# Performance work log

Measured on AMD Instinct MI355X. Metric: run time of the kernel, lower is better.

## Reference

```python
import jax, jax.numpy as jnp
import numpy as np

B = 2
NUM_CLS = 20
NUM_DIM = 256
H = W = 448
FH = FW = 28
K_TOP = 25


def _l2norm(x, eps=1e-12):
    # matches torch F.normalize(dim=1): x / max(||x||, eps); zero rows stay zero
    return x / jnp.maximum(jnp.linalg.norm(x, axis=-1, keepdims=True), eps)


def setup_inputs():
    key = jax.random.key(0)
    k1, k2, k3, k4 = jax.random.split(key, 4)
    fmap = jax.random.normal(k1, (B, NUM_DIM, FH, FW), jnp.float32)
    cam = jax.random.uniform(k2, (B, NUM_CLS, H, W), jnp.float32)
    cls_label = jax.random.randint(k3, (B, NUM_CLS), 0, 2).astype(jnp.float32)
    proj_weight = jax.random.normal(k4, (NUM_CLS, NUM_DIM), jnp.float32) * 0.02
    feature_contrast = jnp.zeros((NUM_CLS, NUM_DIM), jnp.float32)
    return {"fmap": fmap, "cam": cam, "cls_label": cls_label,
            "proj_weight": proj_weight, "feature_contrast": feature_contrast,
            "hig_thre": 0.7, "low_thre": 0.25, "bg_thre": 0.5}


def _forward(fmap, cam, cls_label, proj_weight, feature_contrast, hig_thre, low_thre, bg_thre):
    b, c, h, w = cam.shape
    d = fmap.shape[1]
    dt = fmap.dtype

    # ---- pseudo-label generation (vectorized over b,h,w) ----
    valid_cam = cls_label[:, :, None, None] * cam                       # [B,C,H,W]
    top2_v, top2_i = jax.lax.top_k(jnp.moveaxis(valid_cam, 1, -1), 2)   # [B,H,W,2]
    top1, second = top2_v[..., 0], top2_v[..., 1]
    pseudo = top2_i[..., 0] + 1
    pseudo = jnp.where(top1 < hig_thre, 255, pseudo)
    pseudo = jnp.where(top1 < low_thre, 0, pseudo)
    pseudo = jnp.where(top1 < bg_thre, 0, pseudo)
    pseudo = jnp.where((top1 - second < 0.3) & (top1 > hig_thre), 255, pseudo)

    # ---- upsample features (bilinear, align_corners=False) ----
    fmap_up = jax.image.resize(fmap, (b, d, h, w), 'bilinear')
    fmap_flat = fmap_up.reshape(b, d, h * w)                            # [B,D,HW]
    pseudo_flat = pseudo.reshape(b, h * w)                              # [B,HW]

    # ---- per-class features, both branches computed densely then selected ----
    cls_ids = jnp.arange(c) + 1
    mask = (pseudo_flat[:, None, :] == cls_ids[None, :, None]).astype(dt)  # [B,C,HW]
    counts = mask.sum(-1)                                                  # [B,C]
    feat_mask = jnp.einsum('bcp,bdp->bcd', mask, fmap_flat) / jnp.maximum(counts, 1.0)[:, :, None]
    _, top_idx = jax.lax.top_k(valid_cam.reshape(b, c, h * w), K_TOP)      # [B,C,25]
    gathered = jnp.take_along_axis(fmap_flat[:, None, :, :], top_idx[:, :, None, :], axis=-1)  # [B,C,D,25]
    feat_topk = gathered.mean(-1)                                          # [B,C,D]
    present = cls_label > 0.5                                              # [B,C] bool
    fsm = jnp.where((counts == 0.0)[:, :, None], feat_topk, feat_mask) * present[:, :, None]

    eye_f = jnp.eye(c, dtype=dt)
    eye_b = jnp.eye(c, dtype=bool)

    # ---- sequential per-sample loop (EMA memory bank carried across batch) ----
    def step(carry, xs):
        fc, loss_cls, loss_ccf = carry
        fsm_i, present_i = xs                                    # [C,D], [C]
        fsm_n = _l2norm(fsm_i)
        fc_n = _l2norm(jax.lax.stop_gradient(fc))
        cos = jnp.clip(jnp.abs(fsm_n @ fc_n.T), 1e-5, 1.0 - 1e-5)  # [C,C]
        ident = jnp.diag(present_i.astype(dt))
        loss_ccf = loss_ccf - (ident * jnp.log(cos) + (1.0 - ident) * jnp.log1p(-cos)).mean()
        off_max = jnp.where(eye_b, -jnp.inf, cos).max(axis=1)      # max over j != c
        qualify = present_i & (off_max < 0.6)                      # [C] bool
        p = jax.nn.softmax(fsm_i @ proj_weight.T, axis=-1)         # [C,C]
        logp = jnp.maximum(jnp.log(p), -100.0)
        log1mp = jnp.maximum(jnp.log1p(-p), -100.0)
        term = -(eye_f * logp + (1.0 - eye_f) * log1mp).mean(axis=-1)  # BCE(softmax, onehot) per class
        loss_cls = loss_cls + jnp.sum(jnp.where(qualify, term, 0.0))
        n = qualify.sum().astype(dt)
        loss_cls = jnp.where(n > 0, loss_cls / jnp.maximum(n, 1.0), loss_cls)
        fc = jnp.where(qualify[:, None], 0.95 * fc + 0.05 * jax.lax.stop_gradient(fsm_i), fc)
        return (fc, loss_cls, loss_ccf), None

    zero = jnp.asarray(0.0, dt)
    (_, loss_cls, loss_ccf), _ = jax.lax.scan(step, (feature_contrast, zero, zero), (fsm, present))
    return loss_ccf + loss_cls


def reference(fmap, cam, cls_label, proj_weight, feature_contrast, hig_thre, low_thre, bg_thre):
    return _forward(fmap, cam, cls_label, proj_weight, feature_contrast, hig_thre, low_thre, bg_thre)
```

## Files before the change

### kernel.cpp

```cpp
#include <hip/hip_runtime.h>
#include <cstdint>

#define HW 200704
#define IMG_W 448
#define NCLS 20
#define NDIM 256
#define NB2 784
#define LK 260

#define ASYNC_COPY16(gp, lp)                                                   \
  __builtin_amdgcn_global_load_lds(                                            \
      (const __attribute__((address_space(1))) void*)(gp),                     \
      (__attribute__((address_space(3))) void*)(lp), 16, 0, 0)

__global__ __launch_bounds__(256) void k_front(const float* __restrict__ fmap,
                                               float* __restrict__ fmapT,
                                               const float* __restrict__ cam,
                                               const float* __restrict__ cls_label,
                                               const float* __restrict__ hig_p,
                                               const float* __restrict__ low_p,
                                               const float* __restrict__ bg_p,
                                               float* __restrict__ W) {
  __shared__ float sT[NCLS][256];
  __shared__ int presList[NCLS];
  __shared__ int sNP;
  int tid = threadIdx.x;

  if (blockIdx.x >= 2 * NB2) {
    float (*tile)[33] = (float (*)[33]) & sT[0][0];
    int blk = blockIdx.x - 2 * NB2;
    int b = blk / 200;
    int t = blk % 200;
    int dT = t / 25, sT2 = t % 25;
    int ty = tid >> 5, tx = tid & 31;
#pragma unroll
    for (int r = 0; r < 4; ++r) {
      int d = dT * 32 + ty + r * 8;
      int s = sT2 * 32 + tx;
      if (s < 784) tile[ty + r * 8][tx] = fmap[((size_t)(b * 256 + d)) * 784 + s];
    }
    __syncthreads();
#pragma unroll
    for (int r = 0; r < 4; ++r) {
      int s = sT2 * 32 + ty + r * 8;
      int d = dT * 32 + tx;
      if (s < 784) fmapT[((size_t)(b * 784 + s)) * 256 + d] = tile[tx][ty + r * 8];
    }
    return;
  }

  int b = blockIdx.x / NB2;
  int blkInB = blockIdx.x % NB2;
  int pix0 = blkInB * 256;
  int wave = tid >> 6, lane = tid & 63;

  if (tid < 64) {
    bool pres = (tid < NCLS) && (cls_label[b * NCLS + tid] != 0.0f);
    unsigned long long pm = __ballot(pres);
    if (pres) presList[(int)__popcll(pm & ((1ull << tid) - 1ull))] = tid;
    if (tid == 0) sNP = (int)__popcll(pm);
  }
  __syncthreads();
  int np = sNP;
  const float* camb = cam + (size_t)b * NCLS * HW + pix0;

  for (int k = wave; k < np; k += 4)
    ASYNC_COPY16(camb + (size_t)presList[k] * HW + lane * 4, &sT[k][0]);
  __syncthreads();

  float top1 = -1.0f, sec = -1.0f;
  int cls1 = 0;
  for (int k = 0; k < np; ++k) {
    float x = sT[k][tid];
    bool gt = x > top1;
    sec = gt ? top1 : fmaxf(sec, fminf(x, top1));
    cls1 = gt ? presList[k] : cls1;
    top1 = gt ? x : top1;
  }
  if (np < NCLS) sec = fmaxf(sec, 0.0f);
  float hig = hig_p[0], low = low_p[0], bg = bg_p[0];
  int pix = pix0 + tid;
  int ps = cls1 + 1;
  if (top1 < hig) ps = 255;
  if (top1 < low) ps = 0;
  if (top1 < bg)  ps = 0;
  if ((top1 - sec < 0.3f) && (top1 > hig)) ps = 255;
  if (ps >= 1 && ps <= NCLS) {
    int cls = ps - 1;
    int y = pix / IMG_W, x = pix % IMG_W;
    float sy = (y + 0.5f) * 0.0625f - 0.5f; sy = fminf(fmaxf(sy, 0.0f), 27.0f);
    float sx = (x + 0.5f) * 0.0625f - 0.5f; sx = fminf(fmaxf(sx, 0.0f), 27.0f);
    int fy0 = (int)sy, fx0 = (int)sx;
    int fy1 = min(fy0 + 1, 27), fx1 = min(fx0 + 1, 27);
    float wy = sy - (float)fy0, wx = sx - (float)fx0;
    float* Wb = W + (size_t)(b * NCLS + cls) * 784;
    atomicAdd(&Wb[fy0 * 28 + fx0], (1.0f - wy) * (1.0f - wx));
    atomicAdd(&Wb[fy0 * 28 + fx1], (1.0f - wy) * wx);
    atomicAdd(&Wb[fy1 * 28 + fx0], wy * (1.0f - wx));
    atomicAdd(&Wb[fy1 * 28 + fx1], wy * wx);
  }
}

__global__ __launch_bounds__(1024) void k_feat_loss(const float* __restrict__ fmapT,
                                                    const float* __restrict__ cam,
                                                    const float* __restrict__ Wg,
                                                    const float* __restrict__ cls_label,
                                                    const float* __restrict__ proj_w,
                                                    const float* __restrict__ fc_init,
                                                    int* __restrict__ done,
                                                    float* __restrict__ fsm_g,
                                                    float* __restrict__ out) {
  __shared__ float sW[784];
  __shared__ float sPart[4][256];
  __shared__ float wv[16]; __shared__ int wi[16];
  __shared__ float selV; __shared__ int selI;
  __shared__ int sTop[25];
  __shared__ int sLast;
  __shared__ float sRed[16];
  __shared__ float sCntf;
  __shared__ float sFsm[NCLS * LK], sFc[NCLS * LK], sPw[NCLS * LK];
  __shared__ float sMat[NCLS * NCLS], sRow[NCLS], sNormI[NCLS], sNormC[NCLS];
  __shared__ int   sZI[NCLS], sZC[NCLS], sQual[NCLS];
  __shared__ float sPres[2][NCLS];
  __shared__ float sScal[2];

  int bc = blockIdx.x;
  int b = bc / NCLS;
  int tid = threadIdx.x;
  int dim = tid & 255, part = tid >> 8;
  bool present = (cls_label[bc] != 0.0f);
  const float* fT = fmapT + (size_t)b * 784 * 256;
  float res = 0.0f;

  if (present) {
    for (int s = tid; s < 784; s += 1024) sW[s] = Wg[(size_t)bc * 784 + s];
    __syncthreads();
    {
      float cs = (tid < 784) ? sW[tid] : 0.0f;
      for (int off = 32; off > 0; off >>= 1) cs += __shfl_xor(cs, off, 64);
      if ((tid & 63) == 0) sRed[tid >> 6] = cs;
      __syncthreads();
      if (tid == 0) {
        float s = 0.0f;
        for (int w = 0; w < 16; ++w) s += sRed[w];
        sCntf = s;
      }
      __syncthreads();
    }
    float cntf = sCntf;
    if (cntf > 0.0f) {
      float a0 = 0.0f, a1 = 0.0f, a2 = 0.0f, a3 = 0.0f;
      int s0 = part * 196;
      for (int s = s0; s < s0 + 196; s += 4) {
        a0 += sW[s]     * fT[(size_t)(s)     * 256 + dim];
        a1 += sW[s + 1] * fT[(size_t)(s + 1) * 256 + dim];
        a2 += sW[s + 2] * fT[(size_t)(s + 2) * 256 + dim];
        a3 += sW[s + 3] * fT[(size_t)(s + 3) * 256 + dim];
      }
      sPart[part][dim] = (a0 + a1) + (a2 + a3);
      __syncthreads();
      if (tid < 256)
        res = ((sPart[0][tid] + sPart[1][tid]) + (sPart[2][tid] + sPart[3][tid]))
              / fmaxf(cntf, 1.0f);
    } else {
      const float* camc = cam + (size_t)bc * HW;
      float lastV = 3.0e38f; int lastI = -1;
      for (int r = 0; r < 25; ++r) {
        float bv = -1.0e30f; int bi = 0x7fffffff;
        for (int p = tid; p < HW; p += 1024) {
          float vv2 = camc[p];
          if (((vv2 < lastV) || (vv2 == lastV && p > lastI)) &&
              ((vv2 > bv) || (vv2 == bv && p < bi))) { bv = vv2; bi = p; }
        }
        for (int off = 32; off > 0; off >>= 1) {
          float ov = __shfl_xor(bv, off, 64);
          int   oi = __shfl_xor(bi, off, 64);
          if (ov > bv || (ov == bv && oi < bi)) { bv = ov; bi = oi; }
        }
        if ((tid & 63) == 0) { wv[tid >> 6] = bv; wi[tid >> 6] = bi; }
        __syncthreads();
        if (tid == 0) {
          for (int w = 1; w < 16; ++w)
            if (wv[w] > bv || (wv[w] == bv && wi[w] < bi)) { bv = wv[w]; bi = wi[w]; }
          selV = bv; selI = bi; sTop[r] = bi;
        }
        __syncthreads();
        lastV = selV; lastI = selI;
      }
      float at = 0.0f;
      for (int r = part; r < 25; r += 4) {
        int p = sTop[r];
        int y = p / IMG_W, x = p % IMG_W;
        float sy = (y + 0.5f) * 0.0625f - 0.5f; sy = fminf(fmaxf(sy, 0.0f), 27.0f);
        float sx = (x + 0.5f) * 0.0625f - 0.5f; sx = fminf(fmaxf(sx, 0.0f), 27.0f);
        int fy0 = (int)sy, fx0 = (int)sx;
        int fy1 = min(fy0 + 1, 27), fx1 = min(fx0 + 1, 27);
        float wy = sy - (float)fy0, wx = sx - (float)fx0;
        at += (1.0f - wy) * (1.0f - wx) * fT[(size_t)(fy0 * 28 + fx0) * 256 + dim]
            + (1.0f - wy) * wx          * fT[(size_t)(fy0 * 28 + fx1) * 256 + dim]
            + wy          * (1.0f - wx) * fT[(size_t)(fy1 * 28 + fx0) * 256 + dim]
            + wy          * wx          * fT[(size_t)(fy1 * 28 + fx1) * 256 + dim];
      }
      sPart[part][dim] = at;
      __syncthreads();
      if (tid < 256)
        res = ((sPart[0][tid] + sPart[1][tid]) + (sPart[2][tid] + sPart[3][tid])) * (1.0f / 25.0f);
    }
  }
  if (tid < 256) fsm_g[(size_t)bc * 256 + tid] = res;
  __syncthreads();
  if (tid == 0) {
    __threadfence();
    int t = atomicAdd(done, 1);
    sLast = (t == 39) ? 1 : 0;
  }
  __syncthreads();
  if (!sLast) return;
  __threadfence();

  for (int idx = tid; idx < NCLS * NDIM; idx += 1024) {
    int r = idx >> 8, d = idx & 255;
    sFc[r * LK + d] = fc_init[idx];
    sPw[r * LK + d] = proj_w[idx];
  }
  if (tid < 40) sPres[tid / NCLS][tid % NCLS] = cls_label[tid];
  if (tid == 0) { sScal[0] = 0.0f; sScal[1] = 0.0f; }
  __syncthreads();

  for (int bb = 0; bb < 2; ++bb) {
    for (int idx = tid; idx < NCLS * NDIM; idx += 1024)
      sFsm[(idx >> 8) * LK + (idx & 255)] = fsm_g[bb * NCLS * NDIM + idx];
    __syncthreads();
    {
      int g = tid >> 3, sub = tid & 7;
      if (g < 40) {
        const float* row = (g < NCLS) ? &sFsm[g * LK] : &sFc[(g - NCLS) * LK];
        float a0 = 0.0f, a1 = 0.0f, a2 = 0.0f, a3 = 0.0f;
        int d0 = sub * 32;
#pragma unroll
        for (int d = d0; d < d0 + 32; d += 8) {
          float4 x = *(const float4*)&row[d];
          float4 y = *(const float4*)&row[d + 4];
          a0 += x.x * x.x + x.y * x.y;
          a1 += x.z * x.z + x.w * x.w;
          a2 += y.x * y.x + y.y * y.y;
          a3 += y.z * y.z + y.w * y.w;
        }
        float s = (a0 + a1) + (a2 + a3);
        s += __shfl_xor(s, 1, 64);
        s += __shfl_xor(s, 2, 64);
        s += __shfl_xor(s, 4, 64);
        if (sub == 0) {
          if (g < NCLS) { sNormI[g] = fmaxf(sqrtf(s), 1e-12f); sZI[g] = (s == 0.0f); }
          else { sNormC[g - NCLS] = fmaxf(sqrtf(s), 1e-12f); sZC[g - NCLS] = (s == 0.0f); }
        }
      }
    }
    __syncthreads();
    {
      int pair = tid >> 1, sub = tid & 1;
      if (pair < 400) {
        int i = pair / NCLS, j = pair % NCLS;
        float c0;
        if (sZI[i] || sZC[j]) c0 = 0.0f;
        else {
          const float* ra = &sFsm[i * LK];
          const float* rb = &sFc[j * LK];
          float a0 = 0.0f, a1 = 0.0f, a2 = 0.0f, a3 = 0.0f;
          int d0 = sub * 128;
          for (int d = d0; d < d0 + 128; d += 8) {
            float4 x  = *(const float4*)&ra[d];
            float4 y  = *(const float4*)&rb[d];
            float4 x2 = *(const float4*)&ra[d + 4];
            float4 y2 = *(const float4*)&rb[d + 4];
            a0 += x.x * y.x + x.y * y.y;
            a1 += x.z * y.z + x.w * y.w;
            a2 += x2.x * y2.x + x2.y * y2.y;
            a3 += x2.z * y2.z + x2.w * y2.w;
          }
          float acc = (a0 + a1) + (a2 + a3);
          acc += __shfl_xor(acc, 1, 64);
          c0 = fabsf(acc / (sNormI[i] * sNormC[j]));
        }
        if (sub == 0) sMat[pair] = fminf(fmaxf(c0, 1e-5f), 1.0f - 1e-5f);
      }
    }
    __syncthreads();
    {
      int i = tid >> 5, jj = tid & 31;
      if (i < NCLS) {
        float pres = (sPres[bb][i] > 0.5f) ? 1.0f : 0.0f;
        float contrib = 0.0f, omv = -3.0e38f;
        if (jj < NCLS) {
          float c0 = sMat[i * NCLS + jj];
          float ident = (jj == i) ? pres : 0.0f;
          contrib = ident * logf(c0) + (1.0f - ident) * log1pf(-c0);
          if (jj != i) omv = c0;
        }
#pragma unroll
        for (int off = 1; off < 32; off <<= 1) {
          contrib += __shfl_xor(contrib, off, 64);
          omv = fmaxf(omv, __shfl_xor(omv, off, 64));
        }
        if (jj == 0) { sRow[i] = contrib; sQual[i] = (pres > 0.5f && omv < 0.6f) ? 1 : 0; }
      }
    }
    __syncthreads();
    if (tid == 0) {
      float s = 0.0f;
      for (int r = 0; r < NCLS; ++r) s += sRow[r];
      sScal[0] -= s / 400.0f;
    }
    __syncthreads();
    {
      int pair = tid >> 1, sub = tid & 1;
      if (pair < 400) {
        int i = pair / NCLS, j = pair % NCLS;
        float acc = 0.0f;
        if (!sZI[i]) {
          const float* ra = &sFsm[i * LK];
          const float* rb = &sPw[j * LK];
          float a0 = 0.0f, a1 = 0.0f, a2 = 0.0f, a3 = 0.0f;
          int d0 = sub * 128;
          for (int d = d0; d < d0 + 128; d += 8) {
            float4 x  = *(const float4*)&ra[d];
            float4 y  = *(const float4*)&rb[d];
            float4 x2 = *(const float4*)&ra[d + 4];
            float4 y2 = *(const float4*)&rb[d + 4];
            a0 += x.x * y.x + x.y * y.y;
            a1 += x.z * y.z + x.w * y.w;
            a2 += x2.x * y2.x + x2.y * y2.y;
            a3 += x2.z * y2.z + x2.w * y2.w;
          }
          acc = (a0 + a1) + (a2 + a3);
          acc += __shfl_xor(acc, 1, 64);
        }
        if (sub == 0) sMat[pair] = acc;
      }
    }
    __syncthreads();
    {
      int i = tid >> 5, jj = tid & 31;
      if (i < NCLS) {
        float l = (jj < NCLS) ? sMat[i * NCLS + jj] : -3.0e38f;
        float m = l;
#pragma unroll
        for (int off = 1; off < 32; off <<= 1) m = fmaxf(m, __shfl_xor(m, off, 64));
        float e = (jj < NCLS) ? expf(l - m) : 0.0f;
        float S = e;
#pragma unroll
        for (int off = 1; off < 32; off <<= 1) S += __shfl_xor(S, off, 64);
        float term = 0.0f;
        if (jj < NCLS) {
          float p = e / S;
          term = (jj == i) ? fmaxf(logf(p), -100.0f) : fmaxf(log1pf(-p), -100.0f);
        }
#pragma unroll
        for (int off = 1; off < 32; off <<= 1) term += __shfl_xor(term, off, 64);
        if (jj == 0) sRow[i] = -term / 20.0f;
      }
    }
    __syncthreads();
    if (tid == 0) {
      float add = 0.0f; int nq = 0;
      for (int r = 0; r < NCLS; ++r) if (sQual[r]) { add += sRow[r]; nq++; }
      float lc = sScal[1] + add;
      if (nq > 0) lc = lc / fmaxf((float)nq, 1.0f);
      sScal[1] = lc;
    }
    for (int idx = tid; idx < NCLS * NDIM; idx += 1024) {
      int r = idx >> 8, d = idx & 255;
      if (sQual[r]) sFc[r * LK + d] = 0.95f * sFc[r * LK + d] + 0.05f * sFsm[r * LK + d];
    }
    __syncthreads();
  }
  if (tid == 0) out[0] = sScal[0] + sScal[1];
}

extern "C" void kernel_launch(void* const* d_in, const int* in_sizes, int n_in,
                              void* d_out, int out_size, void* d_ws, size_t ws_size,
                              hipStream_t stream) {
  const float* fmap      = (const float*)d_in[0];
  const float* cam       = (const float*)d_in[1];
  const float* cls_label = (const float*)d_in[2];
  const float* proj_w    = (const float*)d_in[3];
  const float* fc_init   = (const float*)d_in[4];
  const float* hig       = (const float*)d_in[5];
  const float* low       = (const float*)d_in[6];
  const float* bg        = (const float*)d_in[7];
  float* out = (float*)d_out;

  char* ws = (char*)d_ws;
  float* W       = (float*)(ws);
  int*   done    = (int*)  (ws + 125440);
  float* fsm     = (float*)(ws + 125472);
  float* fmapT   = (float*)(ws + 166432);

  hipMemsetAsync(ws, 0, 125472, stream);
  k_front    <<<2 * NB2 + 400,  256, 0, stream>>>(fmap, fmapT, cam, cls_label,
                                                  hig, low, bg, W);
  k_feat_loss<<<           40, 1024, 0, stream>>>(fmapT, cam, W,
                                                  cls_label, proj_w, fc_init, done, fsm, out);
}
```

Before: 132.5 us.

## Split last-block loss tail into separate kernel and batch independent loss work

The per-class feature kernel no longer uses an atomic counter and last-block election to run the loss. A separate single-block loss kernel now runs after it. That kernel loads both batches' class features up front and computes the projection logits, softmax BCE terms and feature norms for both batches in parallel, since none of these depend on the serial feature-contrast update. Only the cosine/contrast step and the qualify-gated update stay sequential over batches. The intent is to shorten the serial tail, at the cost of one extra kernel launch.

```diff
diff --git a/kernel.cpp b/kernel.cpp
--- a/kernel.cpp
+++ b/kernel.cpp
@@ -101,29 +101,18 @@
   }
 }
 
-__global__ __launch_bounds__(1024) void k_feat_loss(const float* __restrict__ fmapT,
-                                                    const float* __restrict__ cam,
-                                                    const float* __restrict__ Wg,
-                                                    const float* __restrict__ cls_label,
-                                                    const float* __restrict__ proj_w,
-                                                    const float* __restrict__ fc_init,
-                                                    int* __restrict__ done,
-                                                    float* __restrict__ fsm_g,
-                                                    float* __restrict__ out) {
+__global__ __launch_bounds__(1024) void k_feat(const float* __restrict__ fmapT,
+                                               const float* __restrict__ cam,
+                                               const float* __restrict__ Wg,
+                                               const float* __restrict__ cls_label,
+                                               float* __restrict__ fsm_g) {
   __shared__ float sW[784];
   __shared__ float sPart[4][256];
   __shared__ float wv[16]; __shared__ int wi[16];
   __shared__ float selV; __shared__ int selI;
   __shared__ int sTop[25];
-  __shared__ int sLast;
   __shared__ float sRed[16];
   __shared__ float sCntf;
-  __shared__ float sFsm[NCLS * LK], sFc[NCLS * LK], sPw[NCLS * LK];
-  __shared__ float sMat[NCLS * NCLS], sRow[NCLS], sNormI[NCLS], sNormC[NCLS];
-  __shared__ int   sZI[NCLS], sZC[NCLS], sQual[NCLS];
-  __shared__ float sPres[2][NCLS];
-  __shared__ float sScal[2];
-
   int bc = blockIdx.x;
   int b = bc / NCLS;
   int tid = threadIdx.x;
@@ -208,16 +197,28 @@
     }
   }
   if (tid < 256) fsm_g[(size_t)bc * 256 + tid] = res;
-  __syncthreads();
-  if (tid == 0) {
-    __threadfence();
-    int t = atomicAdd(done, 1);
-    sLast = (t == 39) ? 1 : 0;
-  }
-  __syncthreads();
-  if (!sLast) return;
-  __threadfence();
-
+}
+
+__global__ __launch_bounds__(1024) void k_loss(const float* __restrict__ fsm_g,
+                                               const float* __restrict__ cls_label,
+                                               const float* __restrict__ proj_w,
+                                               const float* __restrict__ fc_init,
+                                               float* __restrict__ out) {
+  __shared__ float sFsm[2][NCLS * LK];
+  __shared__ float sFc[NCLS * LK], sPw[NCLS * LK];
+  __shared__ float sLogit[2][400], sCos[400];
+  __shared__ float sBCE[2][NCLS], sRow[NCLS];
+  __shared__ float sNormI[2][NCLS], sNormC[NCLS];
+  __shared__ int   sZI[2][NCLS], sZC[NCLS], sQual[NCLS];
+  __shared__ float sPres[2][NCLS];
+  __shared__ float sScal[2];
+  int tid = threadIdx.x;
+
+  for (int idx = tid; idx < 2 * NCLS * NDIM; idx += 1024) {
+    int b = idx / (NCLS * NDIM);
+    int rem = idx - b * NCLS * NDIM;
+    sFsm[b][(rem >> 8) * LK + (rem & 255)] = fsm_g[idx];
+  }
   for (int idx = tid; idx < NCLS * NDIM; idx += 1024) {
     int r = idx >> 8, d = idx & 255;
     sFc[r * LK + d] = fc_init[idx];
@@ -227,14 +228,82 @@
   if (tid == 0) { sScal[0] = 0.0f; sScal[1] = 0.0f; }
   __syncthreads();
 
-  for (int bb = 0; bb < 2; ++bb) {
-    for (int idx = tid; idx < NCLS * NDIM; idx += 1024)
-      sFsm[(idx >> 8) * LK + (idx & 255)] = fsm_g[bb * NCLS * NDIM + idx];
-    __syncthreads();
-    {
+  if (tid < 800) {
+    int b = tid / 400, pi = tid % 400;
+    int i = pi / NCLS, j = pi % NCLS;
+    const float* ra = &sFsm[b][i * LK];
+    const float* rb = &sPw[j * LK];
+    float a0 = 0, a1 = 0, a2 = 0, a3 = 0, a4 = 0, a5 = 0, a6 = 0, a7 = 0;
+    for (int d = 0; d < 256; d += 16) {
+      float4 x0 = *(const float4*)&ra[d],      y0 = *(const float4*)&rb[d];
+      float4 x1 = *(const float4*)&ra[d + 4],  y1 = *(const float4*)&rb[d + 4];
+      float4 x2 = *(const float4*)&ra[d + 8],  y2 = *(const float4*)&rb[d + 8];
+      float4 x3 = *(const float4*)&ra[d + 12], y3 = *(const float4*)&rb[d + 12];
+      a0 += x0.x * y0.x + x0.y * y0.y;  a1 += x0.z * y0.z + x0.w * y0.w;
+      a2 += x1.x * y1.x + x1.y * y1.y;  a3 += x1.z * y1.z + x1.w * y1.w;
+      a4 += x2.x * y2.x + x2.y * y2.y;  a5 += x2.z * y2.z + x2.w * y2.w;
+      a6 += x3.x * y3.x + x3.y * y3.y;  a7 += x3.z * y3.z + x3.w * y3.w;
+    }
+    sLogit[b][pi] = ((a0 + a1) + (a2 + a3)) + ((a4 + a5) + (a6 + a7));
+  }
+  __syncthreads();
+
+  {
+    int g = tid >> 3, sub = tid & 7;
+    if (g < 60) {
+      const float* row = (g < 40) ? &sFsm[g / NCLS][(g % NCLS) * LK] : &sFc[(g - 40) * LK];
+      float a0 = 0.0f, a1 = 0.0f, a2 = 0.0f, a3 = 0.0f;
+      int d0 = sub * 32;
+#pragma unroll
+      for (int d = d0; d < d0 + 32; d += 8) {
+        float4 x = *(const float4*)&row[d];
+        float4 y = *(const float4*)&row[d + 4];
+        a0 += x.x * x.x + x.y * x.y;
+        a1 += x.z * x.z + x.w * x.w;
+        a2 += y.x * y.x + y.y * y.y;
+        a3 += y.z * y.z + y.w * y.w;
+      }
+      float s = (a0 + a1) + (a2 + a3);
+      s += __shfl_xor(s, 1, 64);
+      s += __shfl_xor(s, 2, 64);
+      s += __shfl_xor(s, 4, 64);
+      if (sub == 0) {
+        if (g < 40) { sNormI[g / NCLS][g % NCLS] = fmaxf(sqrtf(s), 1e-12f); sZI[g / NCLS][g % NCLS] = (s == 0.0f); }
+        else { sNormC[g - 40] = fmaxf(sqrtf(s), 1e-12f); sZC[g - 40] = (s == 0.0f); }
+      }
+    }
+  }
+  __syncthreads();
+
+  {
+    int team = tid >> 5, jj = tid & 31;
+    for (int r = team; r < 40; r += 32) {
+      int b = r / NCLS, i = r % NCLS;
+      float l = (jj < NCLS) ? sLogit[b][i * NCLS + jj] : -3.0e38f;
+      float m = l;
+#pragma unroll
+      for (int off = 1; off < 32; off <<= 1) m = fmaxf(m, __shfl_xor(m, off, 64));
+      float e = (jj < NCLS) ? expf(l - m) : 0.0f;
+      float S = e;
+#pragma unroll
+      for (int off = 1; off < 32; off <<= 1) S += __shfl_xor(S, off, 64);
+      float term = 0.0f;
+      if (jj < NCLS) {
+        float p = e / S;
+        term = (jj == i) ? fmaxf(logf(p), -100.0f) : fmaxf(log1pf(-p), -100.0f);
+      }
+#pragma unroll
+      for (int off = 1; off < 32; off <<= 1) term += __shfl_xor(term, off, 64);
+      if (jj == 0) sBCE[b][i] = -term / 20.0f;
+    }
+  }
+  __syncthreads();
+
+  for (int b = 0; b < 2; ++b) {
+    if (b == 1) {
       int g = tid >> 3, sub = tid & 7;
-      if (g < 40) {
-        const float* row = (g < NCLS) ? &sFsm[g * LK] : &sFc[(g - NCLS) * LK];
+      if (g < NCLS) {
+        const float* row = &sFc[g * LK];
         float a0 = 0.0f, a1 = 0.0f, a2 = 0.0f, a3 = 0.0f;
         int d0 = sub * 32;
 #pragma unroll
@@ -250,21 +319,18 @@
         s += __shfl_xor(s, 1, 64);
         s += __shfl_xor(s, 2, 64);
         s += __shfl_xor(s, 4, 64);
-        if (sub == 0) {
-          if (g < NCLS) { sNormI[g] = fmaxf(sqrtf(s), 1e-12f); sZI[g] = (s == 0.0f); }
-          else { sNormC[g - NCLS] = fmaxf(sqrtf(s), 1e-12f); sZC[g - NCLS] = (s == 0.0f); }
-        }
-      }
-    }
-    __syncthreads();
+        if (sub == 0) { sNormC[g] = fmaxf(sqrtf(s), 1e-12f); sZC[g] = (s == 0.0f); }
+      }
+      __syncthreads();
+    }
     {
       int pair = tid >> 1, sub = tid & 1;
       if (pair < 400) {
         int i = pair / NCLS, j = pair % NCLS;
         float c0;
-        if (sZI[i] || sZC[j]) c0 = 0.0f;
+        if (sZI[b][i] || sZC[j]) c0 = 0.0f;
         else {
-          const float* ra = &sFsm[i * LK];
+          const float* ra = &sFsm[b][i * LK];
           const float* rb = &sFc[j * LK];
           float a0 = 0.0f, a1 = 0.0f, a2 = 0.0f, a3 = 0.0f;
           int d0 = sub * 128;
@@ -280,19 +346,19 @@
           }
           float acc = (a0 + a1) + (a2 + a3);
           acc += __shfl_xor(acc, 1, 64);
-          c0 = fabsf(acc / (sNormI[i] * sNormC[j]));
-        }
-        if (sub == 0) sMat[pair] = fminf(fmaxf(c0, 1e-5f), 1.0f - 1e-5f);
+          c0 = fabsf(acc / (sNormI[b][i] * sNormC[j]));
+        }
+        if (sub == 0) sCos[pair] = fminf(fmaxf(c0, 1e-5f), 1.0f - 1e-5f);
       }
     }
     __syncthreads();
     {
       int i = tid >> 5, jj = tid & 31;
       if (i < NCLS) {
-        float pres = (sPres[bb][i] > 0.5f) ? 1.0f : 0.0f;
+        float pres = (sPres[b][i] > 0.5f) ? 1.0f : 0.0f;
         float contrib = 0.0f, omv = -3.0e38f;
         if (jj < NCLS) {
-          float c0 = sMat[i * NCLS + jj];
+          float c0 = sCos[i * NCLS + jj];
           float ident = (jj == i) ? pres : 0.0f;
           contrib = ident * logf(c0) + (1.0f - ident) * log1pf(-c0);
           if (jj != i) omv = c0;
@@ -310,67 +376,15 @@
       float s = 0.0f;
       for (int r = 0; r < NCLS; ++r) s += sRow[r];
       sScal[0] -= s / 400.0f;
-    }
-    __syncthreads();
-    {
-      int pair = tid >> 1, sub = tid & 1;
-      if (pair < 400) {
-        int i = pair / NCLS, j = pair % NCLS;
-        float acc = 0.0f;
-        if (!sZI[i]) {
-          const float* ra = &sFsm[i * LK];
-          const float* rb = &sPw[j * LK];
-          float a0 = 0.0f, a1 = 0.0f, a2 = 0.0f, a3 = 0.0f;
-          int d0 = sub * 128;
-          for (int d = d0; d < d0 + 128; d += 8) {
-            float4 x  = *(const float4*)&ra[d];
-            float4 y  = *(const float4*)&rb[d];
-            float4 x2 = *(const float4*)&ra[d + 4];
-            float4 y2 = *(const float4*)&rb[d + 4];
-            a0 += x.x * y.x + x.y * y.y;
-            a1 += x.z * y.z + x.w * y.w;
-            a2 += x2.x * y2.x + x2.y * y2.y;
-            a3 += x2.z * y2.z + x2.w * y2.w;
-          }
-          acc = (a0 + a1) + (a2 + a3);
-          acc += __shfl_xor(acc, 1, 64);
-        }
-        if (sub == 0) sMat[pair] = acc;
-      }
-    }
-    __syncthreads();
-    {
-      int i = tid >> 5, jj = tid & 31;
-      if (i < NCLS) {
-        float l = (jj < NCLS) ? sMat[i * NCLS + jj] : -3.0e38f;
-        float m = l;
-#pragma unroll
-        for (int off = 1; off < 32; off <<= 1) m = fmaxf(m, __shfl_xor(m, off, 64));
-        float e = (jj < NCLS) ? expf(l - m) : 0.0f;
-        float S = e;
-#pragma unroll
-        for (int off = 1; off < 32; off <<= 1) S += __shfl_xor(S, off, 64);
-        float term = 0.0f;
-        if (jj < NCLS) {
-          float p = e / S;
-          term = (jj == i) ? fmaxf(logf(p), -100.0f) : fmaxf(log1pf(-p), -100.0f);
-        }
-#pragma unroll
-        for (int off = 1; off < 32; off <<= 1) term += __shfl_xor(term, off, 64);
-        if (jj == 0) sRow[i] = -term / 20.0f;
-      }
-    }
-    __syncthreads();
-    if (tid == 0) {
       float add = 0.0f; int nq = 0;
-      for (int r = 0; r < NCLS; ++r) if (sQual[r]) { add += sRow[r]; nq++; }
+      for (int r = 0; r < NCLS; ++r) if (sQual[r]) { add += sBCE[b][r]; nq++; }
       float lc = sScal[1] + add;
       if (nq > 0) lc = lc / fmaxf((float)nq, 1.0f);
       sScal[1] = lc;
     }
     for (int idx = tid; idx < NCLS * NDIM; idx += 1024) {
       int r = idx >> 8, d = idx & 255;
-      if (sQual[r]) sFc[r * LK + d] = 0.95f * sFc[r * LK + d] + 0.05f * sFsm[r * LK + d];
+      if (sQual[r]) sFc[r * LK + d] = 0.95f * sFc[r * LK + d] + 0.05f * sFsm[b][r * LK + d];
     }
     __syncthreads();
   }
@@ -392,13 +406,12 @@
 
   char* ws = (char*)d_ws;
   float* W       = (float*)(ws);
-  int*   done    = (int*)  (ws + 125440);
-  float* fsm     = (float*)(ws + 125472);
-  float* fmapT   = (float*)(ws + 166432);
-
-  hipMemsetAsync(ws, 0, 125472, stream);
-  k_front    <<<2 * NB2 + 400,  256, 0, stream>>>(fmap, fmapT, cam, cls_label,
-                                                  hig, low, bg, W);
-  k_feat_loss<<<           40, 1024, 0, stream>>>(fmapT, cam, W,
-                                                  cls_label, proj_w, fc_init, done, fsm, out);
+  float* fsm     = (float*)(ws + 125440);
+  float* fmapT   = (float*)(ws + 166400);
+
+  hipMemsetAsync(ws, 0, 125440, stream);
+  k_front<<<2 * NB2 + 400,  256, 0, stream>>>(fmap, fmapT, cam, cls_label,
+                                              hig, low, bg, W);
+  k_feat <<<           40, 1024, 0, stream>>>(fmapT, cam, W, cls_label, fsm);
+  k_loss <<<            1, 1024, 0, stream>>>(fsm, cls_label, proj_w, fc_init, out);
 }
```

Measured after the change: 128.1 us. 1.03x faster.
